# Optimization experiments

Measured on AMD Instinct MI355X. Metric: run time of the kernel, lower is better.

The kernel has to match this reference:

```python
import jax, jax.numpy as jnp
import numpy as np

N = 50000
E = 800000
G = 64
H, C = 16, 4  # heads, out_channels per head; H*C = 64


def setup_inputs() -> dict:
    key = jax.random.key(0)
    ks = jax.random.split(key, 16)
    return {
        "x": jax.random.normal(ks[0], (N,), jnp.float32),
        "edge_index": jax.random.randint(ks[1], (2, E), 0, N),
        "edge_attr": jax.random.normal(ks[2], (E,), jnp.float32),
        "batch": jnp.sort(jax.random.randint(ks[3], (N,), 0, G)),
        # GATv2Conv(1 -> 4, heads=16, edge_dim=1, concat=True)
        "Wl": jax.random.normal(ks[4], (1, H * C), jnp.float32) * 0.5,
        "bl": jnp.full((H * C,), 0.01, jnp.float32),
        "Wr": jax.random.normal(ks[5], (1, H * C), jnp.float32) * 0.5,
        "br": jnp.full((H * C,), 0.01, jnp.float32),
        "We": jax.random.normal(ks[6], (1, H * C), jnp.float32) * 0.5,
        "att": jax.random.normal(ks[7], (H, C), jnp.float32) * 0.5,
        "gat_bias": jnp.zeros((H * C,), jnp.float32),
        # GraphNorm(64)
        "gn_w": jnp.ones((H * C,), jnp.float32),
        "gn_b": jnp.zeros((H * C,), jnp.float32),
        "gn_ms": jnp.ones((H * C,), jnp.float32),
        # SAGEConv(64 -> 64, mean aggr, root weight)
        "sage_Wl": jax.random.normal(ks[8], (H * C, 64), jnp.float32) * 0.125,
        "sage_bl": jnp.full((64,), 0.01, jnp.float32),
        "sage_Wr": jax.random.normal(ks[9], (H * C, 64), jnp.float32) * 0.125,
        # MLP head
        "fc1_W": jax.random.normal(ks[10], (128, 2048), jnp.float32) * 0.08,
        "fc1_b": jnp.full((2048,), 0.01, jnp.float32),
        "fc2_W": jax.random.normal(ks[11], (2048, 1024), jnp.float32) * 0.02,
        "fc2_b": jnp.full((1024,), 0.01, jnp.float32),
        "fc3_W": jax.random.normal(ks[12], (1024, 3), jnp.float32) * 0.03,
        "fc3_b": jnp.full((3,), 0.01, jnp.float32),
    }


def reference(x, edge_index, edge_attr, batch, Wl, bl, Wr, br, We, att, gat_bias,
              gn_w, gn_b, gn_ms, sage_Wl, sage_bl, sage_Wr,
              fc1_W, fc1_b, fc2_W, fc2_b, fc3_W, fc3_b):
    src0, dst0 = edge_index[0], edge_index[1]
    x1 = x[:, None]  # [N,1] (torch.unsqueeze(x, -1))
    # ---- GATv2Conv ----
    xl = (x1 @ Wl + bl).reshape(N, H, C)  # source-side (x_j, also the value)
    xr = (x1 @ Wr + br).reshape(N, H, C)  # target-side (x_i)
    # add self loops; fill_value='mean' -> per-node mean of incoming edge_attr
    deg_in = jax.ops.segment_sum(jnp.ones((E,), x.dtype), dst0, num_segments=N)
    loop_attr = jax.ops.segment_sum(edge_attr, dst0, num_segments=N) / jnp.maximum(deg_in, 1.0)
    loops = jnp.arange(N)
    src = jnp.concatenate([src0, loops])
    dst = jnp.concatenate([dst0, loops])
    ea = jnp.concatenate([edge_attr, loop_attr])[:, None]  # [E+N,1]
    e = (ea @ We).reshape(-1, H, C)
    m = jax.nn.leaky_relu(xl[src] + xr[dst] + e, 0.2)  # [E+N,H,C]
    score = jnp.einsum('ehc,hc->eh', m, att)
    smax = jax.ops.segment_max(score, dst, num_segments=N)
    a = jnp.exp(score - smax[dst])
    denom = jax.ops.segment_sum(a, dst, num_segments=N)
    alpha = a / denom[dst]  # segmented softmax over incoming edges
    h = jax.ops.segment_sum(alpha[:, :, None] * xl[src], dst, num_segments=N)
    h = h.reshape(N, H * C) + gat_bias
    h = jax.nn.relu(h)
    # ---- GraphNorm ----
    cnt = jax.ops.segment_sum(jnp.ones((N,), x.dtype), batch, num_segments=G)[:, None]
    mean = jax.ops.segment_sum(h, batch, num_segments=G) / cnt
    o = h - mean[batch] * gn_ms
    var = jax.ops.segment_sum(o * o, batch, num_segments=G) / cnt
    h = gn_w * o / jnp.sqrt(var[batch] + 1e-5) + gn_b
    # ---- SAGEConv (mean aggregation + root weight) ----
    neigh = jax.ops.segment_sum(h[src0], dst0, num_segments=N) / jnp.maximum(deg_in, 1.0)[:, None]
    h = neigh @ sage_Wl + sage_bl + h @ sage_Wr
    h = jax.nn.relu(h)
    # ---- global max + mean pooling, MLP head (eval mode: dropout off) ----
    gmax = jax.ops.segment_max(h, batch, num_segments=G)
    gmean = jax.ops.segment_sum(h, batch, num_segments=G) / cnt
    g = jnp.concatenate([gmax, gmean], axis=1)  # [G, 128]
    g = jax.nn.relu(g @ fc1_W + fc1_b)
    g = jax.nn.relu(g @ fc2_W + fc2_b)
    return g @ fc3_W + fc3_b
```

## Files before the change

### kernel.cpp

```cpp
#include <hip/hip_runtime.h>

#define GG 64
#define HH 16
#define KK 64

__device__ __forceinline__ float bf2f(unsigned short u){
  return __uint_as_float(((unsigned)u) << 16);
}
__device__ __forceinline__ unsigned short f2bf(float f){
  unsigned u = __float_as_uint(f);
  unsigned r = u + 0x7fffu + ((u >> 16) & 1u);
  return (unsigned short)(r >> 16);
}

__global__ void k_zero(int4* __restrict__ p, int nInt4,
                       const int* __restrict__ batch, int N, int* __restrict__ goff){
  int t = blockIdx.x*blockDim.x + threadIdx.x;
  for (int i = t; i < nInt4; i += gridDim.x*blockDim.x)
    p[i] = make_int4(0,0,0,0);
  if (blockIdx.x == 0 && threadIdx.x <= GG){
    int g = threadIdx.x;
    int lo = 0, hi = N;
    while (lo < hi){ int mid = (lo+hi) >> 1; if (batch[mid] < g) lo = mid+1; else hi = mid; }
    goff[g] = lo;
  }
}


__global__ void k_count_rank(const int* __restrict__ ei, int* deg, int* __restrict__ rank, int E){
  int e = blockIdx.x*blockDim.x + threadIdx.x;
  if (e < E) rank[e] = atomicAdd(&deg[ei[E + e]], 1);
}

__global__ void k_scan1(const int* __restrict__ deg, int* __restrict__ bsum, int N){
  int base = blockIdx.x*1024;
  int lim = min(base + 1024, N);
  int s = 0;
  for (int i = base + (int)threadIdx.x; i < lim; i += 256) s += deg[i];
  #pragma unroll
  for (int ofs = 32; ofs >= 1; ofs >>= 1) s += __shfl_down(s, ofs, 64);
  __shared__ int ws[4];
  int lane = threadIdx.x & 63, wv = threadIdx.x >> 6;
  if (lane == 0) ws[wv] = s;
  __syncthreads();
  if (threadIdx.x == 0) bsum[blockIdx.x] = ws[0] + ws[1] + ws[2] + ws[3];
}

__global__ void __launch_bounds__(1024)
k_scan2(int* __restrict__ bsum, int* __restrict__ row_start_N, int NB){
  int t = threadIdx.x;
  int v = (t < NB) ? bsum[t] : 0;
  int lane = t & 63, wv = t >> 6;
  int val = v;
  #pragma unroll
  for (int ofs = 1; ofs < 64; ofs <<= 1){
    int tt = __shfl_up(val, ofs, 64);
    if (lane >= ofs) val += tt;
  }
  __shared__ int ws[16];
  if (lane == 63) ws[wv] = val;
  __syncthreads();
  if (t == 0){
    int run = 0;
    #pragma unroll
    for (int w = 0; w < 16; ++w){ int tmp = ws[w]; ws[w] = run; run += tmp; }
  }
  __syncthreads();
  int excl = ws[wv] + val - v;
  if (t < NB) bsum[t] = excl;
  if (t == NB - 1) *row_start_N = excl + v;
}

__global__ void k_scan3(const int* __restrict__ deg, const int* __restrict__ bsum,
                        int* __restrict__ row_start, int N){
  int b = blockIdx.x;
  int base = b*1024 + (int)threadIdx.x*4;
  int d0 = (base+0 < N) ? deg[base+0] : 0;
  int d1 = (base+1 < N) ? deg[base+1] : 0;
  int d2 = (base+2 < N) ? deg[base+2] : 0;
  int d3 = (base+3 < N) ? deg[base+3] : 0;
  int s = d0 + d1 + d2 + d3;
  int lane = threadIdx.x & 63, wv = threadIdx.x >> 6;
  int val = s;
  #pragma unroll
  for (int ofs = 1; ofs < 64; ofs <<= 1){
    int tt = __shfl_up(val, ofs, 64);
    if (lane >= ofs) val += tt;
  }
  __shared__ int ws[4];
  if (lane == 63) ws[wv] = val;
  __syncthreads();
  if (threadIdx.x == 0){
    int run = 0;
    #pragma unroll
    for (int w = 0; w < 4; ++w){ int tmp = ws[w]; ws[w] = run; run += tmp; }
  }
  __syncthreads();
  int pre = bsum[b] + ws[wv] + val - s;
  if (base+0 < N){ row_start[base+0] = pre; pre += d0; }
  if (base+1 < N){ row_start[base+1] = pre; pre += d1; }
  if (base+2 < N){ row_start[base+2] = pre; pre += d2; }
  if (base+3 < N){ row_start[base+3] = pre; }
}

__global__ void k_scatter(const int* __restrict__ ei, const float* __restrict__ ea,
                          const int* __restrict__ row_start, const int* __restrict__ rank,
                          unsigned* __restrict__ cs, int E){
  int e = blockIdx.x*blockDim.x + threadIdx.x;
  if (e >= E) return;
  int d = ei[E + e];
  int pos = row_start[d] + rank[e];
  cs[pos] = ((unsigned)ei[e] & 0xFFFFu) | ((unsigned)f2bf(ea[e]) << 16);
}

__global__ void k_gat(const float* __restrict__ x, const int* __restrict__ row_start,
                      const unsigned* __restrict__ cs,
                      const float* __restrict__ Wl, const float* __restrict__ bl,
                      const float* __restrict__ Wr, const float* __restrict__ br,
                      const float* __restrict__ We, const float* __restrict__ att,
                      const float* __restrict__ gat_bias, const int* __restrict__ batch,
                      float* __restrict__ h, float* __restrict__ gsum, float* __restrict__ gsum2,
                      int N){
  __shared__ float sh[32][KK+1];
  __shared__ int bg[32];
  int tid = threadIdx.x;
  int t = blockIdx.x*blockDim.x + tid;
  int n   = t >> 3;
  int sub = t & 7;
  int u   = tid >> 3;
  bool act = (n < N);
  if (sub == 0) bg[u] = act ? batch[n] : -1;
  int k0 = sub*8;
  if (act){
    float xd = x[n];
    float wl[8], we[8], at[8], pre[8];
    #pragma unroll
    for (int i = 0; i < 8; ++i){
      int k = k0 + i;
      wl[i] = Wl[k]; we[i] = We[k]; at[i] = att[k];
      pre[i] = bl[k] + fmaf(xd, Wr[k], br[k]);
    }
    int e0 = row_start[n], e1 = row_start[n+1];
    float m[2]  = {-3.4e38f,-3.4e38f};
    float den[2] = {0,0}, S1[2] = {0,0};
    float asum = 0.f;

#define PROC(XS, EAV)                                                        \
    { float xs_ = (XS), ea_ = (EAV);                                         \
      _Pragma("unroll")                                                      \
      for (int hi2 = 0; hi2 < 2; ++hi2){                                     \
        float sc = 0.f;                                                      \
        _Pragma("unroll")                                                    \
        for (int c = 0; c < 4; ++c){                                         \
          int i = hi2*4 + c;                                                 \
          float tt = fmaf(xs_, wl[i], fmaf(ea_, we[i], pre[i]));             \
          tt = (tt > 0.f) ? tt : 0.2f*tt;                                    \
          sc = fmaf(tt, at[i], sc);                                          \
        }                                                                    \
        float nm = fmaxf(m[hi2], sc);                                        \
        float corr = __expf(m[hi2] - nm);                                    \
        float a    = __expf(sc - nm);                                        \
        den[hi2] = den[hi2]*corr + a;                                        \
        S1[hi2]  = S1[hi2] *corr + a*xs_;                                    \
        m[hi2] = nm; } }

    int e = e0;
    for (; e + 3 < e1; e += 4){
      unsigned w0 = cs[e], w1 = cs[e+1], w2 = cs[e+2], w3 = cs[e+3];
      float xs0 = x[w0 & 0xFFFFu], xs1 = x[w1 & 0xFFFFu];
      float xs2 = x[w2 & 0xFFFFu], xs3 = x[w3 & 0xFFFFu];
      float ea0 = bf2f((unsigned short)(w0 >> 16)), ea1 = bf2f((unsigned short)(w1 >> 16));
      float ea2 = bf2f((unsigned short)(w2 >> 16)), ea3 = bf2f((unsigned short)(w3 >> 16));
      asum += (ea0 + ea1) + (ea2 + ea3);
      PROC(xs0, ea0);
      PROC(xs1, ea1);
      PROC(xs2, ea2);
      PROC(xs3, ea3);
    }
    for (; e < e1; ++e){
      unsigned w0 = cs[e];
      float xs0 = x[w0 & 0xFFFFu], ea0 = bf2f((unsigned short)(w0 >> 16));
      asum += ea0;
      PROC(xs0, ea0);
    }
    {
      float degf = (float)(e1 - e0);
      float eav = asum / fmaxf(degf, 1.0f);
      PROC(xd, eav);
    }
#undef PROC
    #pragma unroll
    for (int hi2 = 0; hi2 < 2; ++hi2){
      float r = S1[hi2] / den[hi2];
      float4 o;
      #pragma unroll
      for (int c = 0; c < 4; ++c){
        int i = hi2*4 + c, k = k0 + i;
        float v = fmaxf(fmaf(wl[i], r, bl[k] + gat_bias[k]), 0.f);
        ((float*)&o)[c] = v;
        sh[u][k] = v;
      }
      *(float4*)(h + (size_t)n*KK + k0 + hi2*4) = o;
    }
  } else {
    #pragma unroll
    for (int i = 0; i < 8; ++i) sh[u][k0+i] = 0.f;
  }
  __syncthreads();
  int ch = tid & 63, slice = tid >> 6;
  int cg = -2; float rs = 0.f, rs2 = 0.f;
  for (int uu = slice*8; uu < slice*8 + 8; ++uu){
    int g = bg[uu];
    if (g != cg){
      if (cg >= 0){ atomicAdd(&gsum[cg*KK + ch], rs); atomicAdd(&gsum2[cg*KK + ch], rs2); }
      cg = g; rs = 0.f; rs2 = 0.f;
    }
    if (g >= 0){ float v = sh[uu][ch]; rs += v; rs2 += v*v; }
  }
  if (cg >= 0){ atomicAdd(&gsum[cg*KK + ch], rs); atomicAdd(&gsum2[cg*KK + ch], rs2); }
}

__global__ void k_norm(float* __restrict__ h, unsigned short* __restrict__ hb,
                       const int* __restrict__ batch,
                       const float* __restrict__ gsum, const float* __restrict__ gsum2,
                       const int* __restrict__ goff,
                       const float* __restrict__ gn_w, const float* __restrict__ gn_b,
                       const float* __restrict__ gn_ms, int N){
  int t = blockIdx.x*blockDim.x + threadIdx.x;
  if (t >= N*16) return;
  int n = t >> 4, q = t & 15;
  int b = batch[n];
  float c = fmaxf((float)(goff[b+1] - goff[b]), 1.0f);
  float inv = 1.0f / c;
  float4 hv = *(float4*)(h + (size_t)n*KK + q*4);
  float ov[4];
  #pragma unroll
  for (int i = 0; i < 4; ++i){
    int k = q*4 + i;
    float mean = gsum[b*KK + k]*inv;
    float eh2  = gsum2[b*KK + k]*inv;
    float ms = gn_ms[k];
    float var = eh2 - 2.f*ms*mean*mean + ms*ms*mean*mean;
    float sc = gn_w[k] * __frsqrt_rn(var + 1e-5f);
    float sh = gn_b[k] - sc*mean*ms;
    ov[i] = fmaf(sc, ((float*)&hv)[i], sh);
  }
  *(float4*)(h + (size_t)n*KK + q*4) = make_float4(ov[0], ov[1], ov[2], ov[3]);
  ushort4 bv;
  bv.x = f2bf(ov[0]); bv.y = f2bf(ov[1]); bv.z = f2bf(ov[2]); bv.w = f2bf(ov[3]);
  *(ushort4*)(hb + (size_t)n*KK + q*4) = bv;
}

__global__ void k_sage(const float* __restrict__ h, const unsigned short* __restrict__ hb,
                       const int* __restrict__ row_start, const unsigned* __restrict__ cs,
                       const float* __restrict__ Wl, const float* __restrict__ bln,
                       const float* __restrict__ Wr, const int* __restrict__ batch,
                       unsigned* __restrict__ gmaxu, float* __restrict__ gsumP, int N){
  __shared__ float snm[16][KK], shn[16][KK];
  __shared__ int bg[16];
  const ushort4* hb4 = (const ushort4*)hb;
  int tid = threadIdx.x;
  int u = tid >> 4;
  int q = tid & 15;
  int n = blockIdx.x*16 + u;
  if (tid < 16) bg[tid] = (blockIdx.x*16 + tid < N) ? batch[blockIdx.x*16 + tid] : -1;
  if (n < N){
    int e0 = row_start[n], e1 = row_start[n+1];
    float a0=0.f,a1=0.f,a2=0.f,a3=0.f;
    float b0=0.f,b1=0.f,b2=0.f,b3=0.f;
    int e = e0;
    for (; e + 7 < e1; e += 8){
      int s0 = cs[e]   & 0xFFFF, s1 = cs[e+1] & 0xFFFF, s2 = cs[e+2] & 0xFFFF, s3 = cs[e+3] & 0xFFFF;
      int s4 = cs[e+4] & 0xFFFF, s5 = cs[e+5] & 0xFFFF, s6 = cs[e+6] & 0xFFFF, s7 = cs[e+7] & 0xFFFF;
      ushort4 v0 = hb4[(size_t)s0*16 + q];
      ushort4 v1 = hb4[(size_t)s1*16 + q];
      ushort4 v2 = hb4[(size_t)s2*16 + q];
      ushort4 v3 = hb4[(size_t)s3*16 + q];
      ushort4 v4 = hb4[(size_t)s4*16 + q];
      ushort4 v5 = hb4[(size_t)s5*16 + q];
      ushort4 v6 = hb4[(size_t)s6*16 + q];
      ushort4 v7 = hb4[(size_t)s7*16 + q];
      a0 += bf2f(v0.x); a1 += bf2f(v0.y); a2 += bf2f(v0.z); a3 += bf2f(v0.w);
      b0 += bf2f(v1.x); b1 += bf2f(v1.y); b2 += bf2f(v1.z); b3 += bf2f(v1.w);
      a0 += bf2f(v2.x); a1 += bf2f(v2.y); a2 += bf2f(v2.z); a3 += bf2f(v2.w);
      b0 += bf2f(v3.x); b1 += bf2f(v3.y); b2 += bf2f(v3.z); b3 += bf2f(v3.w);
      a0 += bf2f(v4.x); a1 += bf2f(v4.y); a2 += bf2f(v4.z); a3 += bf2f(v4.w);
      b0 += bf2f(v5.x); b1 += bf2f(v5.y); b2 += bf2f(v5.z); b3 += bf2f(v5.w);
      a0 += bf2f(v6.x); a1 += bf2f(v6.y); a2 += bf2f(v6.z); a3 += bf2f(v6.w);
      b0 += bf2f(v7.x); b1 += bf2f(v7.y); b2 += bf2f(v7.z); b3 += bf2f(v7.w);
    }
    if (e + 3 < e1){
      int s0 = cs[e] & 0xFFFF, s1 = cs[e+1] & 0xFFFF, s2 = cs[e+2] & 0xFFFF, s3 = cs[e+3] & 0xFFFF;
      ushort4 v0 = hb4[(size_t)s0*16 + q];
      ushort4 v1 = hb4[(size_t)s1*16 + q];
      ushort4 v2 = hb4[(size_t)s2*16 + q];
      ushort4 v3 = hb4[(size_t)s3*16 + q];
      a0 += bf2f(v0.x); a1 += bf2f(v0.y); a2 += bf2f(v0.z); a3 += bf2f(v0.w);
      b0 += bf2f(v1.x); b1 += bf2f(v1.y); b2 += bf2f(v1.z); b3 += bf2f(v1.w);
      a0 += bf2f(v2.x); a1 += bf2f(v2.y); a2 += bf2f(v2.z); a3 += bf2f(v2.w);
      b0 += bf2f(v3.x); b1 += bf2f(v3.y); b2 += bf2f(v3.z); b3 += bf2f(v3.w);
      e += 4;
    }
    for (; e < e1; ++e){
      ushort4 v0 = hb4[(size_t)(cs[e] & 0xFFFF)*16 + q];
      a0 += bf2f(v0.x); a1 += bf2f(v0.y); a2 += bf2f(v0.z); a3 += bf2f(v0.w);
    }
    float dg = fmaxf((float)(e1 - e0), 1.0f);
    float inv = 1.0f/dg;
    float4 nm = make_float4((a0+b0)*inv, (a1+b1)*inv, (a2+b2)*inv, (a3+b3)*inv);
    *(float4*)&snm[u][q*4] = nm;
    *(float4*)&shn[u][q*4] = *(const float4*)(h + (size_t)n*KK + q*4);
  }
  __syncthreads();
  int j = tid & 63, u0 = tid >> 6;
  float acc[4];
  #pragma unroll
  for (int p = 0; p < 4; ++p) acc[p] = bln[j];
  for (int k = 0; k < KK; ++k){
    float wlv = Wl[k*KK + j], wrv = Wr[k*KK + j];
    #pragma unroll
    for (int p = 0; p < 4; ++p){
      int un = u0 + p*4;
      acc[p] = fmaf(snm[un][k], wlv, acc[p]);
      acc[p] = fmaf(shn[un][k], wrv, acc[p]);
    }
  }
  __syncthreads();
  #pragma unroll
  for (int p = 0; p < 4; ++p)
    snm[u0 + p*4][j] = fmaxf(acc[p], 0.f);
  __syncthreads();
  if (tid < 64){
    int cg = -2; float rmax = 0.f, rsum = 0.f;
    for (int uu = 0; uu < 16; ++uu){
      int g = bg[uu];
      if (g != cg){
        if (cg >= 0){
          atomicMax(&gmaxu[cg*KK + tid], __float_as_uint(rmax));
          atomicAdd(&gsumP[cg*KK + tid], rsum);
        }
        cg = g; rmax = 0.f; rsum = 0.f;
      }
      if (g >= 0){ float v = snm[uu][tid]; rmax = fmaxf(rmax, v); rsum += v; }
    }
    if (cg >= 0){
      atomicMax(&gmaxu[cg*KK + tid], __float_as_uint(rmax));
      atomicAdd(&gsumP[cg*KK + tid], rsum);
    }
  }
}


__global__ void k_fc1(const unsigned* __restrict__ gmaxu, const float* __restrict__ gsumP,
                      const int* __restrict__ goff,
                      const float* __restrict__ W, const float* __restrict__ b,
                      float* __restrict__ out){
  __shared__ float sin[128];
  int g = blockIdx.y, jt = blockIdx.x;
  int tid = threadIdx.x;
  if (tid < 128){
    float c = fmaxf((float)(goff[g+1] - goff[g]), 1.0f);
    sin[tid] = (tid < 64) ? __uint_as_float(gmaxu[g*64 + tid])
                          : gsumP[g*64 + (tid-64)] / c;
  }
  __syncthreads();
  int j = jt*256 + tid;
  float acc = b[j];
  #pragma unroll 16
  for (int k = 0; k < 128; ++k)
    acc = fmaf(sin[k], W[(size_t)k*2048 + j], acc);
  out[(size_t)g*2048 + j] = fmaxf(acc, 0.f);
}

__global__ void k_fc2a(const float* __restrict__ in, const float* __restrict__ W,
                       float* __restrict__ partial){
  __shared__ float sin[64][128];
  int jt = blockIdx.x, ks = blockIdx.y;
  int k0 = ks*128;
  int tid = threadIdx.x;
  for (int idx = tid; idx < 64*128; idx += 256){
    int g = idx >> 7, k = idx & 127;
    sin[g][k] = in[(size_t)g*2048 + k0 + k];
  }
  __syncthreads();
  int j = tid & 63, gs = tid >> 6;
  const float* Wp = W + (size_t)k0*1024 + jt*64 + j;
  float acc[16];
  #pragma unroll
  for (int p = 0; p < 16; ++p) acc[p] = 0.f;
  for (int k = 0; k < 128; ++k){
    float w = Wp[(size_t)k*1024];
    #pragma unroll
    for (int p = 0; p < 16; ++p)
      acc[p] = fmaf(sin[gs*16 + p][k], w, acc[p]);
  }
  #pragma unroll
  for (int p = 0; p < 16; ++p){
    int g = gs*16 + p;
    partial[((size_t)ks*64 + g)*1024 + jt*64 + j] = acc[p];
  }
}

__global__ void k_fc2red(const float* __restrict__ partial, const float* __restrict__ b,
                         float* __restrict__ out){
  int i = blockIdx.x*blockDim.x + threadIdx.x;
  int g = i >> 10, j = i & 1023;
  float s = b[j];
  #pragma unroll
  for (int ks = 0; ks < 16; ++ks)
    s += partial[((size_t)ks*64 + g)*1024 + j];
  out[i] = fmaxf(s, 0.f);
}

__global__ void k_fc3(const float* __restrict__ in, const float* __restrict__ W,
                      const float* __restrict__ b, float* __restrict__ out, int nOut){
  int w = (blockIdx.x*blockDim.x + threadIdx.x) >> 6;
  int lane = threadIdx.x & 63;
  if (w >= GG*nOut) return;
  int g = w / nOut, j = w - g*nOut;
  const float* row = in + (size_t)g*1024;
  float acc = 0.f;
  #pragma unroll
  for (int k = lane; k < 1024; k += 64)
    acc = fmaf(row[k], W[(size_t)k*nOut + j], acc);
  #pragma unroll
  for (int ofs = 32; ofs >= 1; ofs >>= 1)
    acc += __shfl_down(acc, ofs, 64);
  if (lane == 0) out[w] = acc + b[j];
}

extern "C" void kernel_launch(void* const* d_in, const int* in_sizes, int n_in,
                              void* d_out, int out_size, void* d_ws, size_t ws_size,
                              hipStream_t stream) {
  const float* x        = (const float*)d_in[0];
  const int*   ei       = (const int*)d_in[1];
  const float* ea       = (const float*)d_in[2];
  const int*   batch    = (const int*)d_in[3];
  const float* Wl       = (const float*)d_in[4];
  const float* bl       = (const float*)d_in[5];
  const float* Wr       = (const float*)d_in[6];
  const float* br       = (const float*)d_in[7];
  const float* We       = (const float*)d_in[8];
  const float* att      = (const float*)d_in[9];
  const float* gat_bias = (const float*)d_in[10];
  const float* gn_w     = (const float*)d_in[11];
  const float* gn_b     = (const float*)d_in[12];
  const float* gn_ms    = (const float*)d_in[13];
  const float* sage_Wl  = (const float*)d_in[14];
  const float* sage_bl  = (const float*)d_in[15];
  const float* sage_Wr  = (const float*)d_in[16];
  const float* fc1_W    = (const float*)d_in[17];
  const float* fc1_b    = (const float*)d_in[18];
  const float* fc2_W    = (const float*)d_in[19];
  const float* fc2_b    = (const float*)d_in[20];
  const float* fc3_W    = (const float*)d_in[21];
  const float* fc3_b    = (const float*)d_in[22];

  const int N = in_sizes[0];
  const int E = in_sizes[1] / 2;
  const int NB = (N + 1023) / 1024;

  char* ws = (char*)d_ws;
  size_t off = 0;
  auto alloc = [&](size_t bytes){ void* p = ws + off; off += (bytes + 255) & ~(size_t)255; return p; };

  int*      deg_i  = (int*)alloc((size_t)N*4);
  float*    gsum   = (float*)alloc(GG*KK*4);
  float*    gsum2  = (float*)alloc(GG*KK*4);
  unsigned* gmaxu  = (unsigned*)alloc(GG*KK*4);
  float*    gsumP  = (float*)alloc(GG*KK*4);
  size_t zero_bytes = off;
  int*   rank      = (int*)alloc((size_t)E*4);
  int*   bsum      = (int*)alloc((size_t)NB*4);
  int*   row_start = (int*)alloc((size_t)(N+1)*4);
  int*   goff      = (int*)alloc((GG+1)*4);
  unsigned* csp    = (unsigned*)alloc((size_t)E*4);
  float* h         = (float*)alloc((size_t)N*KK*4);
  unsigned short* hb = (unsigned short*)alloc((size_t)N*KK*2);
  float* out1      = (float*)alloc((size_t)GG*2048*4);
  float* out2      = (float*)alloc((size_t)GG*1024*4);
  float* partial   = (float*)alloc((size_t)16*GG*1024*4);
  (void)ws_size; (void)n_in; (void)out_size;

  const int B = 256;
  {
    int nInt4 = (int)(zero_bytes >> 4);
    int blocks = min((nInt4 + B - 1)/B, 256);
    k_zero <<<blocks, B, 0, stream>>>((int4*)d_ws, nInt4, batch, N, goff);
  }
  k_count_rank<<<(E+B-1)/B, B, 0, stream>>>(ei, deg_i, rank, E);
  k_scan1  <<<NB, B, 0, stream>>>(deg_i, bsum, N);
  k_scan2  <<<1, 1024, 0, stream>>>(bsum, row_start + N, NB);
  k_scan3  <<<NB, B, 0, stream>>>(deg_i, bsum, row_start, N);
  k_scatter<<<(E+B-1)/B, B, 0, stream>>>(ei, ea, row_start, rank, csp, E);
  k_gat    <<<((size_t)N*8+B-1)/B, B, 0, stream>>>(x, row_start, csp,
                                                   Wl, bl, Wr, br, We, att, gat_bias,
                                                   batch, h, gsum, gsum2, N);
  k_norm   <<<((size_t)N*16+B-1)/B, B, 0, stream>>>(h, hb, batch, gsum, gsum2, goff,
                                                    gn_w, gn_b, gn_ms, N);
  k_sage   <<<(N+15)/16, B, 0, stream>>>(h, hb, row_start, csp, sage_Wl, sage_bl, sage_Wr,
                                         batch, gmaxu, gsumP, N);
  {
    dim3 grid(8, GG);
    k_fc1  <<<grid, 256, 0, stream>>>(gmaxu, gsumP, goff, fc1_W, fc1_b, out1);
  }
  {
    dim3 grid(16, 16);
    k_fc2a <<<grid, 256, 0, stream>>>(out1, fc2_W, partial);
  }
  k_fc2red <<<(GG*1024+B-1)/B, B, 0, stream>>>(partial, fc2_b, out2);
  k_fc3    <<<(GG*3*64+B-1)/B, B, 0, stream>>>(out2, fc3_W, fc3_b, (float*)d_out, 3);
}
```

Measured before the change: 178.0 us.

## Split node edge loops across strips in GAT and SAGE, fuse scan passes

The GAT kernel now gives each node 32 threads: 4 edge strips times 8 channel groups. The strips' online-softmax partial states (max, denominator, weighted sum) are merged with xor shuffles. The SAGE kernel likewise splits each node's neighbor gather across two strips, handles 8 nodes per block, and combines the strips with a shuffle. The first two scan kernels are fused into one using a last-block-done atomic counter, which removes a launch. The aim is more parallelism per node for the latency-bound irregular gathers, at the cost of more threads, shuffle-merge overhead and less per-block reuse of the SAGE weight loads.

```diff
diff --git a/kernel.cpp b/kernel.cpp
--- a/kernel.cpp
+++ b/kernel.cpp
@@ -32,43 +32,47 @@
   if (e < E) rank[e] = atomicAdd(&deg[ei[E + e]], 1);
 }
 
-__global__ void k_scan1(const int* __restrict__ deg, int* __restrict__ bsum, int N){
+__global__ void k_scanA(const int* __restrict__ deg, int* __restrict__ bsum,
+                        int* __restrict__ counter, int* __restrict__ row_start_N,
+                        int N, int NB){
+  int tid = threadIdx.x;
   int base = blockIdx.x*1024;
   int lim = min(base + 1024, N);
   int s = 0;
-  for (int i = base + (int)threadIdx.x; i < lim; i += 256) s += deg[i];
+  for (int i = base + tid; i < lim; i += 256) s += deg[i];
   #pragma unroll
   for (int ofs = 32; ofs >= 1; ofs >>= 1) s += __shfl_down(s, ofs, 64);
   __shared__ int ws[4];
-  int lane = threadIdx.x & 63, wv = threadIdx.x >> 6;
+  __shared__ int lastflag;
+  int lane = tid & 63, wv = tid >> 6;
   if (lane == 0) ws[wv] = s;
   __syncthreads();
-  if (threadIdx.x == 0) bsum[blockIdx.x] = ws[0] + ws[1] + ws[2] + ws[3];
-}
-
-__global__ void __launch_bounds__(1024)
-k_scan2(int* __restrict__ bsum, int* __restrict__ row_start_N, int NB){
-  int t = threadIdx.x;
-  int v = (t < NB) ? bsum[t] : 0;
-  int lane = t & 63, wv = t >> 6;
-  int val = v;
-  #pragma unroll
-  for (int ofs = 1; ofs < 64; ofs <<= 1){
-    int tt = __shfl_up(val, ofs, 64);
-    if (lane >= ofs) val += tt;
-  }
-  __shared__ int ws[16];
-  if (lane == 63) ws[wv] = val;
-  __syncthreads();
-  if (t == 0){
+  if (tid == 0){
+    bsum[blockIdx.x] = ws[0] + ws[1] + ws[2] + ws[3];
+    __threadfence();
+    int d = atomicAdd(counter, 1);
+    lastflag = (d == NB - 1);
+  }
+  __syncthreads();
+  if (!lastflag) return;
+  __threadfence();
+  if (NB <= 64){
+    if (tid < 64){
+      int v = (tid < NB) ? bsum[tid] : 0;
+      int val = v;
+      #pragma unroll
+      for (int ofs = 1; ofs < 64; ofs <<= 1){
+        int tt = __shfl_up(val, ofs, 64);
+        if ((tid & 63) >= ofs) val += tt;
+      }
+      if (tid < NB) bsum[tid] = val - v;
+      if (tid == NB - 1) *row_start_N = val;
+    }
+  } else if (tid == 0){
     int run = 0;
-    #pragma unroll
-    for (int w = 0; w < 16; ++w){ int tmp = ws[w]; ws[w] = run; run += tmp; }
-  }
-  __syncthreads();
-  int excl = ws[wv] + val - v;
-  if (t < NB) bsum[t] = excl;
-  if (t == NB - 1) *row_start_N = excl + v;
+    for (int i = 0; i < NB; ++i){ int tmp = bsum[i]; bsum[i] = run; run += tmp; }
+    *row_start_N = run;
+  }
 }
 
 __global__ void k_scan3(const int* __restrict__ deg, const int* __restrict__ bsum,
@@ -121,29 +125,33 @@
                       const float* __restrict__ gat_bias, const int* __restrict__ batch,
                       float* __restrict__ h, float* __restrict__ gsum, float* __restrict__ gsum2,
                       int N){
-  __shared__ float sh[32][KK+1];
-  __shared__ int bg[32];
+  __shared__ float sh[8][KK+1];
+  __shared__ int bg[8];
   int tid = threadIdx.x;
   int t = blockIdx.x*blockDim.x + tid;
-  int n   = t >> 3;
-  int sub = t & 7;
-  int u   = tid >> 3;
+  int n     = t >> 5;
+  int l5    = t & 31;
+  int strip = l5 >> 3;
+  int sub   = l5 & 7;
+  int u     = tid >> 5;
   bool act = (n < N);
-  if (sub == 0) bg[u] = act ? batch[n] : -1;
+  if (l5 == 0) bg[u] = act ? batch[n] : -1;
   int k0 = sub*8;
+  float wl[8], we[8], at[8], pre[8];
+  float m[2]  = {-3.4e38f,-3.4e38f};
+  float den[2] = {0,0}, S1[2] = {0,0};
+  float asum = 0.f;
+  float xd = 0.f;
+  int e0 = 0, e1 = 0;
   if (act){
-    float xd = x[n];
-    float wl[8], we[8], at[8], pre[8];
+    xd = x[n];
     #pragma unroll
     for (int i = 0; i < 8; ++i){
       int k = k0 + i;
       wl[i] = Wl[k]; we[i] = We[k]; at[i] = att[k];
       pre[i] = bl[k] + fmaf(xd, Wr[k], br[k]);
     }
-    int e0 = row_start[n], e1 = row_start[n+1];
-    float m[2]  = {-3.4e38f,-3.4e38f};
-    float den[2] = {0,0}, S1[2] = {0,0};
-    float asum = 0.f;
+    e0 = row_start[n]; e1 = row_start[n+1];
 
 #define PROC(XS, EAV)                                                        \
     { float xs_ = (XS), ea_ = (EAV);                                         \
@@ -164,52 +172,66 @@
         S1[hi2]  = S1[hi2] *corr + a*xs_;                                    \
         m[hi2] = nm; } }
 
-    int e = e0;
-    for (; e + 3 < e1; e += 4){
-      unsigned w0 = cs[e], w1 = cs[e+1], w2 = cs[e+2], w3 = cs[e+3];
+    int e = e0 + strip;
+    for (; e + 4 < e1; e += 8){
+      unsigned w0 = cs[e], w1 = cs[e+4];
       float xs0 = x[w0 & 0xFFFFu], xs1 = x[w1 & 0xFFFFu];
-      float xs2 = x[w2 & 0xFFFFu], xs3 = x[w3 & 0xFFFFu];
       float ea0 = bf2f((unsigned short)(w0 >> 16)), ea1 = bf2f((unsigned short)(w1 >> 16));
-      float ea2 = bf2f((unsigned short)(w2 >> 16)), ea3 = bf2f((unsigned short)(w3 >> 16));
-      asum += (ea0 + ea1) + (ea2 + ea3);
+      asum += ea0 + ea1;
       PROC(xs0, ea0);
       PROC(xs1, ea1);
-      PROC(xs2, ea2);
-      PROC(xs3, ea3);
-    }
-    for (; e < e1; ++e){
+    }
+    for (; e < e1; e += 4){
       unsigned w0 = cs[e];
       float xs0 = x[w0 & 0xFFFFu], ea0 = bf2f((unsigned short)(w0 >> 16));
       asum += ea0;
       PROC(xs0, ea0);
     }
-    {
-      float degf = (float)(e1 - e0);
-      float eav = asum / fmaxf(degf, 1.0f);
-      PROC(xd, eav);
-    }
-#undef PROC
+  }
+  #pragma unroll
+  for (int ofs = 8; ofs <= 16; ofs <<= 1){
     #pragma unroll
     for (int hi2 = 0; hi2 < 2; ++hi2){
-      float r = S1[hi2] / den[hi2];
-      float4 o;
+      float mo = __shfl_xor(m[hi2],  ofs, 64);
+      float dn = __shfl_xor(den[hi2], ofs, 64);
+      float s1 = __shfl_xor(S1[hi2],  ofs, 64);
+      float nm = fmaxf(m[hi2], mo);
+      float c1 = __expf(m[hi2] - nm);
+      float c2 = __expf(mo - nm);
+      den[hi2] = den[hi2]*c1 + dn*c2;
+      S1[hi2]  = S1[hi2] *c1 + s1*c2;
+      m[hi2] = nm;
+    }
+    asum += __shfl_xor(asum, ofs, 64);
+  }
+  if (act){
+    float degf = (float)(e1 - e0);
+    float eav = asum / fmaxf(degf, 1.0f);
+    PROC(xd, eav);
+#undef PROC
+    if (strip == 0){
       #pragma unroll
-      for (int c = 0; c < 4; ++c){
-        int i = hi2*4 + c, k = k0 + i;
-        float v = fmaxf(fmaf(wl[i], r, bl[k] + gat_bias[k]), 0.f);
-        ((float*)&o)[c] = v;
-        sh[u][k] = v;
+      for (int hi2 = 0; hi2 < 2; ++hi2){
+        float r = S1[hi2] / den[hi2];
+        float4 o;
+        #pragma unroll
+        for (int c = 0; c < 4; ++c){
+          int i = hi2*4 + c, k = k0 + i;
+          float v = fmaxf(fmaf(wl[i], r, bl[k] + gat_bias[k]), 0.f);
+          ((float*)&o)[c] = v;
+          sh[u][k] = v;
+        }
+        *(float4*)(h + (size_t)n*KK + k0 + hi2*4) = o;
       }
-      *(float4*)(h + (size_t)n*KK + k0 + hi2*4) = o;
-    }
-  } else {
+    }
+  } else if (strip == 0){
     #pragma unroll
     for (int i = 0; i < 8; ++i) sh[u][k0+i] = 0.f;
   }
   __syncthreads();
   int ch = tid & 63, slice = tid >> 6;
   int cg = -2; float rs = 0.f, rs2 = 0.f;
-  for (int uu = slice*8; uu < slice*8 + 8; ++uu){
+  for (int uu = slice*2; uu < slice*2 + 2; ++uu){
     int g = bg[uu];
     if (g != cg){
       if (cg >= 0){ atomicAdd(&gsum[cg*KK + ch], rs); atomicAdd(&gsum2[cg*KK + ch], rs2); }
@@ -256,41 +278,24 @@
                        const float* __restrict__ Wl, const float* __restrict__ bln,
                        const float* __restrict__ Wr, const int* __restrict__ batch,
                        unsigned* __restrict__ gmaxu, float* __restrict__ gsumP, int N){
-  __shared__ float snm[16][KK], shn[16][KK];
-  __shared__ int bg[16];
+  __shared__ float snm[8][KK], shn[8][KK];
+  __shared__ int bg[8];
   const ushort4* hb4 = (const ushort4*)hb;
   int tid = threadIdx.x;
-  int u = tid >> 4;
-  int q = tid & 15;
-  int n = blockIdx.x*16 + u;
-  if (tid < 16) bg[tid] = (blockIdx.x*16 + tid < N) ? batch[blockIdx.x*16 + tid] : -1;
+  int u     = tid >> 5;
+  int l5    = tid & 31;
+  int strip = l5 >> 4;
+  int q     = l5 & 15;
+  int n = blockIdx.x*8 + u;
+  if (tid < 8) bg[tid] = (blockIdx.x*8 + tid < N) ? batch[blockIdx.x*8 + tid] : -1;
   if (n < N){
     int e0 = row_start[n], e1 = row_start[n+1];
     float a0=0.f,a1=0.f,a2=0.f,a3=0.f;
     float b0=0.f,b1=0.f,b2=0.f,b3=0.f;
-    int e = e0;
-    for (; e + 7 < e1; e += 8){
-      int s0 = cs[e]   & 0xFFFF, s1 = cs[e+1] & 0xFFFF, s2 = cs[e+2] & 0xFFFF, s3 = cs[e+3] & 0xFFFF;
-      int s4 = cs[e+4] & 0xFFFF, s5 = cs[e+5] & 0xFFFF, s6 = cs[e+6] & 0xFFFF, s7 = cs[e+7] & 0xFFFF;
-      ushort4 v0 = hb4[(size_t)s0*16 + q];
-      ushort4 v1 = hb4[(size_t)s1*16 + q];
-      ushort4 v2 = hb4[(size_t)s2*16 + q];
-      ushort4 v3 = hb4[(size_t)s3*16 + q];
-      ushort4 v4 = hb4[(size_t)s4*16 + q];
-      ushort4 v5 = hb4[(size_t)s5*16 + q];
-      ushort4 v6 = hb4[(size_t)s6*16 + q];
-      ushort4 v7 = hb4[(size_t)s7*16 + q];
-      a0 += bf2f(v0.x); a1 += bf2f(v0.y); a2 += bf2f(v0.z); a3 += bf2f(v0.w);
-      b0 += bf2f(v1.x); b1 += bf2f(v1.y); b2 += bf2f(v1.z); b3 += bf2f(v1.w);
-      a0 += bf2f(v2.x); a1 += bf2f(v2.y); a2 += bf2f(v2.z); a3 += bf2f(v2.w);
-      b0 += bf2f(v3.x); b1 += bf2f(v3.y); b2 += bf2f(v3.z); b3 += bf2f(v3.w);
-      a0 += bf2f(v4.x); a1 += bf2f(v4.y); a2 += bf2f(v4.z); a3 += bf2f(v4.w);
-      b0 += bf2f(v5.x); b1 += bf2f(v5.y); b2 += bf2f(v5.z); b3 += bf2f(v5.w);
-      a0 += bf2f(v6.x); a1 += bf2f(v6.y); a2 += bf2f(v6.z); a3 += bf2f(v6.w);
-      b0 += bf2f(v7.x); b1 += bf2f(v7.y); b2 += bf2f(v7.z); b3 += bf2f(v7.w);
-    }
-    if (e + 3 < e1){
-      int s0 = cs[e] & 0xFFFF, s1 = cs[e+1] & 0xFFFF, s2 = cs[e+2] & 0xFFFF, s3 = cs[e+3] & 0xFFFF;
+    int e = e0 + strip;
+    for (; e + 6 < e1; e += 8){
+      int s0 = cs[e]   & 0xFFFF, s1 = cs[e+2] & 0xFFFF;
+      int s2 = cs[e+4] & 0xFFFF, s3 = cs[e+6] & 0xFFFF;
       ushort4 v0 = hb4[(size_t)s0*16 + q];
       ushort4 v1 = hb4[(size_t)s1*16 + q];
       ushort4 v2 = hb4[(size_t)s2*16 + q];
@@ -299,27 +304,32 @@
       b0 += bf2f(v1.x); b1 += bf2f(v1.y); b2 += bf2f(v1.z); b3 += bf2f(v1.w);
       a0 += bf2f(v2.x); a1 += bf2f(v2.y); a2 += bf2f(v2.z); a3 += bf2f(v2.w);
       b0 += bf2f(v3.x); b1 += bf2f(v3.y); b2 += bf2f(v3.z); b3 += bf2f(v3.w);
-      e += 4;
-    }
-    for (; e < e1; ++e){
+    }
+    for (; e < e1; e += 2){
       ushort4 v0 = hb4[(size_t)(cs[e] & 0xFFFF)*16 + q];
       a0 += bf2f(v0.x); a1 += bf2f(v0.y); a2 += bf2f(v0.z); a3 += bf2f(v0.w);
     }
-    float dg = fmaxf((float)(e1 - e0), 1.0f);
-    float inv = 1.0f/dg;
-    float4 nm = make_float4((a0+b0)*inv, (a1+b1)*inv, (a2+b2)*inv, (a3+b3)*inv);
-    *(float4*)&snm[u][q*4] = nm;
-    *(float4*)&shn[u][q*4] = *(const float4*)(h + (size_t)n*KK + q*4);
+    a0 += b0; a1 += b1; a2 += b2; a3 += b3;
+    a0 += __shfl_xor(a0, 16, 64);
+    a1 += __shfl_xor(a1, 16, 64);
+    a2 += __shfl_xor(a2, 16, 64);
+    a3 += __shfl_xor(a3, 16, 64);
+    if (strip == 0){
+      float dg = fmaxf((float)(e1 - e0), 1.0f);
+      float inv = 1.0f/dg;
+      *(float4*)&snm[u][q*4] = make_float4(a0*inv, a1*inv, a2*inv, a3*inv);
+      *(float4*)&shn[u][q*4] = *(const float4*)(h + (size_t)n*KK + q*4);
+    }
   }
   __syncthreads();
   int j = tid & 63, u0 = tid >> 6;
-  float acc[4];
-  #pragma unroll
-  for (int p = 0; p < 4; ++p) acc[p] = bln[j];
+  float acc[2];
+  #pragma unroll
+  for (int p = 0; p < 2; ++p) acc[p] = bln[j];
   for (int k = 0; k < KK; ++k){
     float wlv = Wl[k*KK + j], wrv = Wr[k*KK + j];
     #pragma unroll
-    for (int p = 0; p < 4; ++p){
+    for (int p = 0; p < 2; ++p){
       int un = u0 + p*4;
       acc[p] = fmaf(snm[un][k], wlv, acc[p]);
       acc[p] = fmaf(shn[un][k], wrv, acc[p]);
@@ -327,12 +337,12 @@
   }
   __syncthreads();
   #pragma unroll
-  for (int p = 0; p < 4; ++p)
+  for (int p = 0; p < 2; ++p)
     snm[u0 + p*4][j] = fmaxf(acc[p], 0.f);
   __syncthreads();
   if (tid < 64){
     int cg = -2; float rmax = 0.f, rsum = 0.f;
-    for (int uu = 0; uu < 16; ++uu){
+    for (int uu = 0; uu < 8; ++uu){
       int g = bg[uu];
       if (g != cg){
         if (cg >= 0){
@@ -469,6 +479,7 @@
   float*    gsum2  = (float*)alloc(GG*KK*4);
   unsigned* gmaxu  = (unsigned*)alloc(GG*KK*4);
   float*    gsumP  = (float*)alloc(GG*KK*4);
+  int*      counter= (int*)alloc(256);
   size_t zero_bytes = off;
   int*   rank      = (int*)alloc((size_t)E*4);
   int*   bsum      = (int*)alloc((size_t)NB*4);
@@ -489,17 +500,16 @@
     k_zero <<<blocks, B, 0, stream>>>((int4*)d_ws, nInt4, batch, N, goff);
   }
   k_count_rank<<<(E+B-1)/B, B, 0, stream>>>(ei, deg_i, rank, E);
-  k_scan1  <<<NB, B, 0, stream>>>(deg_i, bsum, N);
-  k_scan2  <<<1, 1024, 0, stream>>>(bsum, row_start + N, NB);
+  k_scanA  <<<NB, B, 0, stream>>>(deg_i, bsum, counter, row_start + N, N, NB);
   k_scan3  <<<NB, B, 0, stream>>>(deg_i, bsum, row_start, N);
   k_scatter<<<(E+B-1)/B, B, 0, stream>>>(ei, ea, row_start, rank, csp, E);
-  k_gat    <<<((size_t)N*8+B-1)/B, B, 0, stream>>>(x, row_start, csp,
-                                                   Wl, bl, Wr, br, We, att, gat_bias,
-                                                   batch, h, gsum, gsum2, N);
+  k_gat    <<<((size_t)N*32+B-1)/B, B, 0, stream>>>(x, row_start, csp,
+                                                    Wl, bl, Wr, br, We, att, gat_bias,
+                                                    batch, h, gsum, gsum2, N);
   k_norm   <<<((size_t)N*16+B-1)/B, B, 0, stream>>>(h, hb, batch, gsum, gsum2, goff,
                                                     gn_w, gn_b, gn_ms, N);
-  k_sage   <<<(N+15)/16, B, 0, stream>>>(h, hb, row_start, csp, sage_Wl, sage_bl, sage_Wr,
-                                         batch, gmaxu, gsumP, N);
+  k_sage   <<<(N+7)/8, B, 0, stream>>>(h, hb, row_start, csp, sage_Wl, sage_bl, sage_Wr,
+                                       batch, gmaxu, gsumP, N);
   {
     dim3 grid(8, GG);
     k_fc1  <<<grid, 256, 0, stream>>>(gmaxu, gsumP, goff, fc1_W, fc1_b, out1);
```

Measured after the change: 218.0 us. 22.5% more time.
